# Kernel tuning notes

Hardware: AMD Instinct MI355X
Metric: run time of the kernel (lower is better)

## Reference

```python
import jax, jax.numpy as jnp
import numpy as np

CLUSTERS = 128
ITERATIONS = 10
TOPK = 32
NEG = -1e7


def setup_inputs() -> dict:
    key = jax.random.key(0)
    k1, k2, k3, k4 = jax.random.split(key, 4)
    N, L, H, E = 2, 2048, 8, 64
    BITS = 32
    return {
        "queries": jax.random.normal(k1, (N, L, H, E), dtype=jnp.float32),
        "keys": jax.random.normal(k2, (N, L, H, E), dtype=jnp.float32),
        "values": jax.random.normal(k3, (N, L, H, E), dtype=jnp.float32),
        "planes": jax.random.normal(k4, (BITS, E + 1), dtype=jnp.float32),
    }


def _cluster(bits, C, iterations):
    # bits: [N,H,L,B] in {0,1}. Lloyd k-means under Hamming distance.
    N, H, L, B = bits.shape
    init_idx = (np.arange(C) * L) // C
    cent = bits[:, :, init_idx, :]  # [N,H,C,B]
    for _ in range(iterations):
        # hamming(b,c) = b.(1-c) + (1-b).c
        d = (jnp.einsum('nhlb,nhcb->nhlc', bits, 1.0 - cent)
             + jnp.einsum('nhlb,nhcb->nhlc', 1.0 - bits, cent))
        assign = jnp.argmin(d, axis=-1)                      # [N,H,L]
        oh = jax.nn.one_hot(assign, C, dtype=jnp.float32)    # [N,H,L,C]
        cnt = oh.sum(axis=2)                                 # [N,H,C]
        sums = jnp.einsum('nhlc,nhlb->nhcb', oh, bits)
        new = (sums / jnp.maximum(cnt, 1.0)[..., None] >= 0.5).astype(jnp.float32)
        cent = jnp.where((cnt > 0.0)[..., None], new, cent)
    d = (jnp.einsum('nhlb,nhcb->nhlc', bits, 1.0 - cent)
         + jnp.einsum('nhlb,nhcb->nhlc', 1.0 - bits, cent))
    assign = jnp.argmin(d, axis=-1)
    oh = jax.nn.one_hot(assign, C, dtype=jnp.float32)
    cnt = oh.sum(axis=2)
    return assign, oh, cnt


def _forward(queries, keys, values, planes):
    # to [N,H,L,E]
    Q = jnp.transpose(queries, (0, 2, 1, 3))
    K = jnp.transpose(keys, (0, 2, 1, 3))
    V = jnp.transpose(values, (0, 2, 1, 3))
    N, H, L, E = Q.shape
    S = K.shape[2]
    temp = 1.0 / np.sqrt(E)

    # --- hash queries with random hyperplanes (bias column: hash_bias=True) ---
    x = jnp.concatenate([Q, jnp.ones(Q.shape[:-1] + (1,), Q.dtype)], axis=-1)
    bits = (jnp.einsum('nhle,be->nhlb', x, planes) > 0).astype(jnp.float32)

    # --- cluster queries (Lloyd on hamming distance over hash bits) ---
    assign, oh, cnt = _cluster(bits, CLUSTERS, ITERATIONS)

    # --- per-cluster centroid queries (mean over members) ---
    Qg = jnp.einsum('nhlc,nhle->nhce', oh, Q) / jnp.maximum(cnt, 1.0)[..., None]

    # --- top-k keys per cluster ---
    QKc = jnp.einsum('nhce,nhse->nhcs', Qg, K)   # [N,H,C,S]
    k = min(TOPK, S)
    _, tki = jax.lax.top_k(QKc, k)               # [N,H,C,k]

    # broadcast each cluster's top-k indices to its member queries
    idx_q = jnp.take_along_axis(
        tki, jnp.broadcast_to(assign[:, :, :, None], (N, H, L, k)), axis=2)  # [N,H,L,k]

    gather = jax.vmap(jax.vmap(lambda a, i: a[i]))
    K_sel = gather(K, idx_q)                     # [N,H,L,k,E]
    V_sel = gather(V, idx_q)                     # [N,H,L,k,E]

    qk = jnp.einsum('nhle,nhlke->nhlk', Q, K_sel)
    future = idx_q > jnp.arange(L)[None, None, :, None]   # causal: key pos > query pos
    qk = jnp.where(future, NEG, qk)
    A = jax.nn.softmax(temp * qk, axis=-1)
    A = A * (1.0 - future.astype(A.dtype))
    out = jnp.einsum('nhlk,nhlkd->nhld', A, V_sel)
    return jnp.transpose(out, (0, 2, 1, 3))      # [N,L,H,D]


def reference(queries, keys, values, planes):
    return _forward(queries, keys, values, planes)
```

## Files before the change

### kernel.cpp

```cpp
#include <hip/hip_runtime.h>
#include <math.h>

#define NB 2
#define HB 8
#define LB 2048
#define EB 64
#define BITSN 32
#define CLN 128
#define ITERS 10
#define TOPKN 32
#define NEGV -10000000.0f

typedef unsigned long long u64;
typedef unsigned int u32;

#define PART_NH16 (33 * 64)
#define PART_ITER16 (NB * HB * PART_NH16)
#define PART_TOTAL16 (ITERS * PART_ITER16)
#define BITS_BLOCKS 4096
#define ZBLOCKS ((PART_TOTAL16 + 255) / 256)

__global__ __launch_bounds__(256) void bits_zero_kernel(const float* __restrict__ q,
                                                        const float* __restrict__ planes,
                                                        u32* __restrict__ bits,
                                                        u32* __restrict__ zbuf) {
    int tid = threadIdx.x;
    int bid = blockIdx.x;
    if (bid >= BITS_BLOCKS) {
        int i = (bid - BITS_BLOCKS) * 256 + tid;
        if (i < PART_TOTAL16) zbuf[i] = 0u;
        return;
    }
    int wave = tid >> 6;
    int lane = tid & 63;
    int b = lane & 31;
    int which = lane >> 5;
    int qi = bid * 8 + wave * 2 + which;
    int l = qi & (LB - 1);
    int nh = qi / LB;
    int h = nh & (HB - 1);
    int n = nh / HB;
    const float* qrow = q + (((long long)n * LB + l) * HB + h) * EB;
    const float* prow = planes + b * (EB + 1);
    double acc = (double)prow[EB];
    #pragma unroll 8
    for (int e = 0; e < EB; ++e) acc += (double)qrow[e] * (double)prow[e];
    unsigned long long m = __ballot(acc > 0.0);
    if (b == 0) {
        bits[qi] = (u32)(which ? (m >> 32) : (m & 0xffffffffULL));
    }
}

__global__ __launch_bounds__(256) void kmeans_iter_kernel(const u32* __restrict__ bits,
                                                          const u32* __restrict__ part_prev,
                                                          u32* __restrict__ part_cur,
                                                          const u32* __restrict__ cent_prev_g,
                                                          u32* __restrict__ cent_cur_g,
                                                          int it) {
    __shared__ u32 cent[CLN];
    __shared__ int hist[33 * 128];
    int tid = threadIdx.x;
    int bid = blockIdx.x;
    int nh = bid >> 3;
    int tile = bid & 7;
    int lane = tid & 63;

    for (int i = tid; i < 33 * 128; i += 256) hist[i] = 0;
    if (tid < CLN) {
        u32 cv;
        if (it == 0) {
            cv = bits[nh * LB + tid * (LB / CLN)];
        } else {
            const u32* pp = part_prev + nh * PART_NH16;
            int sh = (tid & 1) * 16;
            int cnt = (int)((pp[32 * 64 + (tid >> 1)] >> sh) & 0xffffu);
            u32 nb = 0u;
            #pragma unroll
            for (int j = 0; j < BITSN; ++j) {
                int s = (int)((pp[j * 64 + (tid >> 1)] >> sh) & 0xffffu);
                if (2 * s >= cnt) nb |= (1u << j);
            }
            cv = (cnt > 0) ? nb : cent_prev_g[nh * CLN + tid];
        }
        cent[tid] = cv;
        if (tile == 0) cent_cur_g[nh * CLN + tid] = cv;
    }
    __syncthreads();

    int l = tile * 256 + tid;
    u32 bv = bits[nh * LB + l];

    u32 clo = cent[lane], chi = cent[lane + 64];
    u32 best = 0x7fffffffu;
    #pragma unroll 16
    for (int c = 0; c < 64; ++c) {
        u32 cc = (u32)__builtin_amdgcn_readlane((int)clo, c);
        u32 key = ((u32)__popc(bv ^ cc) << 7) | (u32)c;
        best = (key < best) ? key : best;
    }
    #pragma unroll 16
    for (int c = 0; c < 64; ++c) {
        u32 cc = (u32)__builtin_amdgcn_readlane((int)chi, c);
        u32 key = ((u32)__popc(bv ^ cc) << 7) | (u32)(64 + c);
        best = (key < best) ? key : best;
    }
    int bc = (int)(best & 127u);

    atomicAdd(&hist[32 * 128 + bc], 1);
    u32 bb = bv;
    while (bb) { int j = __ffs(bb) - 1; atomicAdd(&hist[j * 128 + bc], 1); bb &= bb - 1; }
    __syncthreads();

    u32* pc = part_cur + nh * PART_NH16;
    for (int i = tid; i < PART_NH16; i += 256) {
        int j = i >> 6, p = i & 63;
        u32 v = (u32)hist[j * 128 + 2 * p] | ((u32)hist[j * 128 + 2 * p + 1] << 16);
        if (v) atomicAdd(&pc[i], v);
    }
}

__global__ __launch_bounds__(1024) void list_qg_final_kernel(const u32* __restrict__ bits,
                                                             const u32* __restrict__ part_prev,
                                                             const u32* __restrict__ cent_prev_g,
                                                             const float* __restrict__ q,
                                                             int* __restrict__ csort_g,
                                                             int* __restrict__ cnt_g,
                                                             int* __restrict__ ofs_g,
                                                             int* __restrict__ list_g,
                                                             float* __restrict__ qgf) {
    __shared__ u32 cent[CLN];
    __shared__ int cnt[CLN];
    __shared__ int cntw[2][16][CLN];
    __shared__ int ofs[CLN];
    __shared__ unsigned short lists[LB];
    int nh = blockIdx.x;
    int tid = threadIdx.x;
    int w = tid >> 6, lane = tid & 63;

    if (tid < CLN) {
        const u32* pp = part_prev + nh * PART_NH16;
        int sh = (tid & 1) * 16;
        int cn = (int)((pp[32 * 64 + (tid >> 1)] >> sh) & 0xffffu);
        u32 nb = 0u;
        #pragma unroll
        for (int j = 0; j < BITSN; ++j) {
            int s = (int)((pp[j * 64 + (tid >> 1)] >> sh) & 0xffffu);
            if (2 * s >= cn) nb |= (1u << j);
        }
        cent[tid] = (cn > 0) ? nb : cent_prev_g[nh * CLN + tid];
        cnt[tid] = 0;
    }
    for (int i = tid; i < 2 * 16 * CLN; i += 1024) (&cntw[0][0][0])[i] = 0;
    __syncthreads();

    int l0 = tid, l1 = tid + 1024;
    u32 bv0 = bits[nh * LB + l0];
    u32 bv1 = bits[nh * LB + l1];
    u32 clo = cent[lane], chi = cent[lane + 64];
    u32 best0 = 0x7fffffffu, best1 = 0x7fffffffu;
    #pragma unroll 16
    for (int c = 0; c < 64; ++c) {
        u32 cc = (u32)__builtin_amdgcn_readlane((int)clo, c);
        u32 k0 = ((u32)__popc(bv0 ^ cc) << 7) | (u32)c;
        u32 k1 = ((u32)__popc(bv1 ^ cc) << 7) | (u32)c;
        best0 = (k0 < best0) ? k0 : best0;
        best1 = (k1 < best1) ? k1 : best1;
    }
    #pragma unroll 16
    for (int c = 0; c < 64; ++c) {
        u32 cc = (u32)__builtin_amdgcn_readlane((int)chi, c);
        u32 k0 = ((u32)__popc(bv0 ^ cc) << 7) | (u32)(64 + c);
        u32 k1 = ((u32)__popc(bv1 ^ cc) << 7) | (u32)(64 + c);
        best0 = (k0 < best0) ? k0 : best0;
        best1 = (k1 < best1) ? k1 : best1;
    }
    int bc0 = (int)(best0 & 127u);
    int bc1 = (int)(best1 & 127u);
    u64 ltmask = (lane == 0) ? 0ULL : (~0ULL >> (64 - lane));

    int rank0 = 0, rank1 = 0;
    for (int c = 0; c < CLN; ++c) {
        u64 m0 = __ballot(bc0 == c);
        u64 m1 = __ballot(bc1 == c);
        if ((m0 | m1) == 0ULL) continue;
        if (bc0 == c) rank0 = (int)__popcll(m0 & ltmask);
        if (bc1 == c) rank1 = (int)__popcll(m1 & ltmask);
        if (lane == 0) {
            int p0 = (int)__popcll(m0), p1 = (int)__popcll(m1);
            if (p0) cntw[0][w][c] = p0;
            if (p1) cntw[1][w][c] = p1;
            atomicAdd(&cnt[c], p0 + p1);
        }
    }
    __syncthreads();
    if (tid == 0) {
        int run = 0;
        for (int c = 0; c < CLN; ++c) { ofs[c] = run; run += cnt[c]; }
    }
    __syncthreads();
    if (tid < CLN) {
        int c = tid;
        int run = ofs[c];
        #pragma unroll
        for (int g = 0; g < 2; ++g)
            for (int ww = 0; ww < 16; ++ww) {
                int t = cntw[g][ww][c];
                cntw[g][ww][c] = run;
                run += t;
            }
        cnt_g[nh * CLN + c] = cnt[c];
        ofs_g[nh * CLN + c] = ofs[c];
    }
    __syncthreads();
    {
        int p0 = cntw[0][w][bc0] + rank0;
        int p1 = cntw[1][w][bc1] + rank1;
        lists[p0] = (unsigned short)l0;
        lists[p1] = (unsigned short)l1;
        list_g[nh * LB + p0] = l0;
        list_g[nh * LB + p1] = l1;
        csort_g[nh * LB + p0] = bc0;
        csort_g[nh * LB + p1] = bc1;
    }
    __syncthreads();

    int h = nh & (HB - 1);
    int n = nh / HB;
    for (int c = w; c < CLN; c += 16) {
        int cn = cnt[c];
        int o = ofs[c];
        double acc = 0.0;
        for (int i = 0; i < cn; ++i) {
            int l = lists[o + i];
            acc += (double)q[(((long long)n * LB + l) * HB + h) * EB + lane];
        }
        double dcn = (double)(cn > 0 ? cn : 1);
        qgf[(long long)(nh * CLN + c) * EB + lane] = (float)(acc / dcn);
    }
}

__global__ __launch_bounds__(256) void scores_kernel(const float* __restrict__ kk,
                                                     const float* __restrict__ qgf,
                                                     u32* __restrict__ keys) {
    int bid = blockIdx.x;
    int nh = bid >> 4;
    int tile = bid & 15;
    int h = nh & (HB - 1);
    int n = nh / HB;
    int w = threadIdx.x >> 6;
    int lane = threadIdx.x & 63;
    int rl = (w & 1) * 64 + lane;
    int l = tile * 128 + rl;
    int cbase = (w >> 1) * 64;

    const float4* kr4 = (const float4*)(kk + (((long long)n * LB + l) * HB + h) * EB);
    float rr[EB];
    #pragma unroll
    for (int i = 0; i < 16; ++i) {
        float4 t4 = kr4[i];
        rr[4 * i] = t4.x; rr[4 * i + 1] = t4.y; rr[4 * i + 2] = t4.z; rr[4 * i + 3] = t4.w;
    }
    const float* qp0 = qgf + ((long long)nh * CLN + cbase) * EB;
    for (int c = 0; c < 64; ++c) {
        const float4* qp = (const float4*)(qp0 + c * EB);
        float acc = 0.f;
        #pragma unroll
        for (int i = 0; i < 16; ++i) {
            float4 qv = qp[i];
            acc = fmaf(qv.x, rr[4 * i], acc);
            acc = fmaf(qv.y, rr[4 * i + 1], acc);
            acc = fmaf(qv.z, rr[4 * i + 2], acc);
            acc = fmaf(qv.w, rr[4 * i + 3], acc);
        }
        u32 u = __float_as_uint(acc);
        u = ((int)u < 0) ? ~u : (u | 0x80000000u);
        keys[((long long)(nh * CLN + cbase + c)) * LB + l] = u;
    }
}

__global__ __launch_bounds__(64) void topsel_kernel(const u32* __restrict__ keys,
                                                    int* __restrict__ tki_g) {
    int bid = blockIdx.x;
    int lane = threadIdx.x;
    const uint4* kp4 = (const uint4*)(keys + (long long)bid * LB);
    u64 k[32];
    #pragma unroll
    for (int t = 0; t < 8; ++t) {
        uint4 kv = kp4[lane + 64 * t];
        int l0 = (lane + 64 * t) * 4;
        k[4 * t]     = ((u64)kv.x << 32) | (u32)(2047 - l0);
        k[4 * t + 1] = ((u64)kv.y << 32) | (u32)(2047 - (l0 + 1));
        k[4 * t + 2] = ((u64)kv.z << 32) | (u32)(2047 - (l0 + 2));
        k[4 * t + 3] = ((u64)kv.w << 32) | (u32)(2047 - (l0 + 3));
    }
    u64 m0 = k[0], m1 = k[8], m2 = k[16], m3 = k[24];
    #pragma unroll
    for (int t = 1; t < 8; ++t) {
        if (k[t] > m0) m0 = k[t];
        if (k[8 + t] > m1) m1 = k[8 + t];
        if (k[16 + t] > m2) m2 = k[16 + t];
        if (k[24 + t] > m3) m3 = k[24 + t];
    }
    if (m1 > m0) m0 = m1;
    if (m3 > m2) m2 = m3;
    u64 cur = (m2 > m0) ? m2 : m0;

    for (int r = 0; r < TOPKN; ++r) {
        u64 wk = cur;
        #pragma unroll
        for (int off = 1; off < 64; off <<= 1) {
            u64 o = __shfl_xor(wk, off);
            if (o > wk) wk = o;
        }
        if (lane == 0) tki_g[bid * TOPKN + r] = 2047 - (int)(wk & 2047u);
        if (wk == cur) {
            u64 nm = 0ULL;
            #pragma unroll
            for (int t = 0; t < 32; ++t) {
                u64 kt = k[t];
                u64 cand = (kt < wk) ? kt : 0ULL;
                if (cand > nm) nm = cand;
            }
            cur = nm;
        }
    }
}

__global__ __launch_bounds__(256) void attn_kernel(const float* __restrict__ q,
                                                   const float* __restrict__ kk,
                                                   const float* __restrict__ vv,
                                                   const int* __restrict__ list_g,
                                                   const int* __restrict__ csort_g,
                                                   const int* __restrict__ tki_g,
                                                   float* __restrict__ out) {
    int tid = threadIdx.x;
    int wave = tid >> 6, lane = tid & 63;
    int idx = blockIdx.x * 4 + wave;
    int nh = idx >> 11;
    int pos = idx & (LB - 1);
    int l = list_g[nh * LB + pos];
    int c = csort_g[nh * LB + pos];
    int h = nh & (HB - 1);
    int n = nh / HB;
    const int* krow = tki_g + (nh * CLN + c) * TOPKN;
    int j = lane & 31, p = lane >> 5;
    int kidx = krow[j];

    const float* vbase = vv + ((long long)n * LB * HB + h) * EB;
    float vreg[TOPKN];
    #pragma unroll
    for (int jj = 0; jj < TOPKN; ++jj) {
        int kj = __shfl(kidx, jj);
        vreg[jj] = vbase[(long long)kj * (HB * EB) + lane];
    }

    const float4* q4 = (const float4*)(q + (((long long)n * LB + l) * HB + h) * EB) + p * 8;
    const float4* k4 = (const float4*)(kk + (((long long)n * LB + kidx) * HB + h) * EB) + p * 8;
    float part = 0.f;
    #pragma unroll
    for (int i = 0; i < 8; ++i) {
        float4 a = q4[i], b = k4[i];
        part += a.x * b.x + a.y * b.y + a.z * b.z + a.w * b.w;
    }
    float qlo = __shfl(part, j);
    float qhi = __shfl(part, j + 32);
    float qk = qlo + qhi;

    bool future = kidx > l;
    float logit = 0.125f * (future ? NEGV : qk);
    float m = logit;
    #pragma unroll
    for (int off = 16; off; off >>= 1) m = fmaxf(m, __shfl_xor(m, off));
    float ex = expf(logit - m);
    float ssum = ex;
    #pragma unroll
    for (int off = 16; off; off >>= 1) ssum += __shfl_xor(ssum, off);
    float a = future ? 0.f : ex / ssum;

    float oacc = 0.f;
    #pragma unroll
    for (int jj = 0; jj < TOPKN; ++jj) {
        float aj = __shfl(a, jj);
        oacc = fmaf(aj, vreg[jj], oacc);
    }
    out[(((long long)n * LB + l) * HB + h) * EB + lane] = oacc;
}

extern "C" void kernel_launch(void* const* d_in, const int* in_sizes, int n_in,
                              void* d_out, int out_size, void* d_ws, size_t ws_size,
                              hipStream_t stream) {
    const float* q = (const float*)d_in[0];
    const float* k = (const float*)d_in[1];
    const float* v = (const float*)d_in[2];
    const float* planes = (const float*)d_in[3];
    float* out = (float*)d_out;

    const int NQ = NB * HB * LB;
    char* ws = (char*)d_ws;
    u32* bits     = (u32*)(ws);
    int* csort_g  = (int*)(ws + 0x20000);
    int* cnt_g    = (int*)(ws + 0x40000);
    int* ofs_g    = (int*)(ws + 0x42000);
    int* list_g   = (int*)(ws + 0x44000);
    float* qgf    = (float*)(ws + 0x64000);
    int* tki_g    = (int*)(ws + 0xE4000);
    u32* keys     = (u32*)(ws + 0x124000);
    u32* part_all = (u32*)(ws + 0x124000);
    u32* cents0   = (u32*)(ws + 0x124000 + 0x180000);
    u32* cents1   = (u32*)(ws + 0x124000 + 0x182000);

    bits_zero_kernel<<<BITS_BLOCKS + ZBLOCKS, 256, 0, stream>>>(q, planes, bits, part_all);

    for (int it = 0; it < ITERS; ++it) {
        const u32* pp = part_all + (it == 0 ? 0 : (it - 1)) * PART_ITER16;
        u32* pc       = part_all + it * PART_ITER16;
        const u32* cprev = (it & 1) ? cents0 : cents1;
        u32* ccur        = (it & 1) ? cents1 : cents0;
        kmeans_iter_kernel<<<NB * HB * 8, 256, 0, stream>>>(bits, pp, pc, cprev, ccur, it);
    }
    list_qg_final_kernel<<<NB * HB, 1024, 0, stream>>>(
        bits, part_all + 9 * PART_ITER16, cents1, q, csort_g, cnt_g, ofs_g, list_g, qgf);
    scores_kernel<<<NB * HB * 16, 256, 0, stream>>>(k, qgf, keys);
    topsel_kernel<<<NB * HB * CLN, 64, 0, stream>>>(keys, tki_g);
    attn_kernel<<<NQ / 4, 256, 0, stream>>>(q, k, v, list_g, csort_g, tki_g, out);
}
```

Measured before the change: 289.0 us.

## Fuse k-means iterations into one persistent kernel with per-head grid barriers

Replaces the ten per-iteration k-means launches and the final reassignment with a single kernel. The 8 blocks of each head synchronize through global atomic counters between iterations, and all blocks stop early once no assignment changes. Final assignments go to a buffer, so the list kernel no longer recomputes Hamming distances. This removes launch gaps and redundant work, but it relies on all 128 blocks being co-resident for the spin barriers and adds atomic polling.

```diff
diff --git a/kernel.cpp b/kernel.cpp
--- a/kernel.cpp
+++ b/kernel.cpp
@@ -17,8 +17,9 @@
 #define PART_NH16 (33 * 64)
 #define PART_ITER16 (NB * HB * PART_NH16)
 #define PART_TOTAL16 (ITERS * PART_ITER16)
+#define ZN (PART_TOTAL16 + 512)
 #define BITS_BLOCKS 4096
-#define ZBLOCKS ((PART_TOTAL16 + 255) / 256)
+#define ZBLOCKS ((ZN + 255) / 256)
 
 __global__ __launch_bounds__(256) void bits_zero_kernel(const float* __restrict__ q,
                                                         const float* __restrict__ planes,
@@ -28,7 +29,7 @@
     int bid = blockIdx.x;
     if (bid >= BITS_BLOCKS) {
         int i = (bid - BITS_BLOCKS) * 256 + tid;
-        if (i < PART_TOTAL16) zbuf[i] = 0u;
+        if (i < ZN) zbuf[i] = 0u;
         return;
     }
     int wave = tid >> 6;
@@ -51,84 +52,142 @@
     }
 }
 
-__global__ __launch_bounds__(256) void kmeans_iter_kernel(const u32* __restrict__ bits,
-                                                          const u32* __restrict__ part_prev,
-                                                          u32* __restrict__ part_cur,
-                                                          const u32* __restrict__ cent_prev_g,
-                                                          u32* __restrict__ cent_cur_g,
-                                                          int it) {
+__global__ __launch_bounds__(256) void kmeans_single_kernel(const u32* __restrict__ bits,
+                                                            u32* __restrict__ part_all,
+                                                            int* __restrict__ bar,
+                                                            int* __restrict__ chflag,
+                                                            int* __restrict__ assign_g) {
     __shared__ u32 cent[CLN];
     __shared__ int hist[33 * 128];
     int tid = threadIdx.x;
     int bid = blockIdx.x;
     int nh = bid >> 3;
-    int tile = bid & 7;
+    int sub = bid & 7;
     int lane = tid & 63;
-
-    for (int i = tid; i < 33 * 128; i += 256) hist[i] = 0;
-    if (tid < CLN) {
-        u32 cv;
-        if (it == 0) {
-            cv = bits[nh * LB + tid * (LB / CLN)];
-        } else {
-            const u32* pp = part_prev + nh * PART_NH16;
+    int l = sub * 256 + tid;
+    u32 bv = bits[nh * LB + l];
+    int oldbc = -1, bc = 0;
+    bool conv = false;
+
+    for (int it = 0; it < ITERS; ++it) {
+        if (tid < CLN) {
+            u32 cv;
+            if (it == 0) {
+                cv = bits[nh * LB + tid * (LB / CLN)];
+            } else {
+                const u32* pp = part_all + (it - 1) * PART_ITER16 + nh * PART_NH16;
+                int sh = (tid & 1) * 16;
+                u32 wcnt = __hip_atomic_load(&pp[32 * 64 + (tid >> 1)],
+                                             __ATOMIC_RELAXED, __HIP_MEMORY_SCOPE_AGENT);
+                int cnt = (int)((wcnt >> sh) & 0xffffu);
+                u32 nb = 0u;
+                #pragma unroll
+                for (int j = 0; j < BITSN; ++j) {
+                    u32 wv = __hip_atomic_load(&pp[j * 64 + (tid >> 1)],
+                                               __ATOMIC_RELAXED, __HIP_MEMORY_SCOPE_AGENT);
+                    int s = (int)((wv >> sh) & 0xffffu);
+                    if (2 * s >= cnt) nb |= (1u << j);
+                }
+                cv = (cnt > 0) ? nb : cent[tid];
+            }
+            cent[tid] = cv;
+        }
+        for (int i = tid; i < 33 * 128; i += 256) hist[i] = 0;
+        __syncthreads();
+
+        u32 clo = cent[lane], chi = cent[lane + 64];
+        u32 best = 0x7fffffffu;
+        #pragma unroll 16
+        for (int c = 0; c < 64; ++c) {
+            u32 cc = (u32)__builtin_amdgcn_readlane((int)clo, c);
+            u32 key = ((u32)__popc(bv ^ cc) << 7) | (u32)c;
+            best = (key < best) ? key : best;
+        }
+        #pragma unroll 16
+        for (int c = 0; c < 64; ++c) {
+            u32 cc = (u32)__builtin_amdgcn_readlane((int)chi, c);
+            u32 key = ((u32)__popc(bv ^ cc) << 7) | (u32)(64 + c);
+            best = (key < best) ? key : best;
+        }
+        bc = (int)(best & 127u);
+
+        u64 chg = __ballot(bc != oldbc);
+        oldbc = bc;
+        if (lane == 0 && chg) atomicOr(&chflag[nh * 16 + it], 1);
+
+        atomicAdd(&hist[32 * 128 + bc], 1);
+        u32 bb = bv;
+        while (bb) { int j = __ffs(bb) - 1; atomicAdd(&hist[j * 128 + bc], 1); bb &= bb - 1; }
+        __syncthreads();
+
+        u32* pc = part_all + it * PART_ITER16 + nh * PART_NH16;
+        for (int i = tid; i < PART_NH16; i += 256) {
+            int j = i >> 6, p = i & 63;
+            u32 v = (u32)hist[j * 128 + 2 * p] | ((u32)hist[j * 128 + 2 * p + 1] << 16);
+            if (v) atomicAdd(&pc[i], v);
+        }
+
+        __threadfence();
+        __syncthreads();
+        if (tid == 0) {
+            atomicAdd(&bar[nh * 16 + it], 1);
+            while (__hip_atomic_load(&bar[nh * 16 + it], __ATOMIC_ACQUIRE,
+                                     __HIP_MEMORY_SCOPE_AGENT) < 8) {
+                __builtin_amdgcn_s_sleep(2);
+            }
+        }
+        __syncthreads();
+
+        if (__hip_atomic_load(&chflag[nh * 16 + it], __ATOMIC_RELAXED,
+                              __HIP_MEMORY_SCOPE_AGENT) == 0) {
+            conv = true; break;
+        }
+    }
+
+    if (!conv) {
+        if (tid < CLN) {
+            const u32* pp = part_all + 9 * PART_ITER16 + nh * PART_NH16;
             int sh = (tid & 1) * 16;
-            int cnt = (int)((pp[32 * 64 + (tid >> 1)] >> sh) & 0xffffu);
+            u32 wcnt = __hip_atomic_load(&pp[32 * 64 + (tid >> 1)],
+                                         __ATOMIC_RELAXED, __HIP_MEMORY_SCOPE_AGENT);
+            int cnt = (int)((wcnt >> sh) & 0xffffu);
             u32 nb = 0u;
             #pragma unroll
             for (int j = 0; j < BITSN; ++j) {
-                int s = (int)((pp[j * 64 + (tid >> 1)] >> sh) & 0xffffu);
+                u32 wv = __hip_atomic_load(&pp[j * 64 + (tid >> 1)],
+                                           __ATOMIC_RELAXED, __HIP_MEMORY_SCOPE_AGENT);
+                int s = (int)((wv >> sh) & 0xffffu);
                 if (2 * s >= cnt) nb |= (1u << j);
             }
-            cv = (cnt > 0) ? nb : cent_prev_g[nh * CLN + tid];
-        }
-        cent[tid] = cv;
-        if (tile == 0) cent_cur_g[nh * CLN + tid] = cv;
-    }
-    __syncthreads();
-
-    int l = tile * 256 + tid;
-    u32 bv = bits[nh * LB + l];
-
-    u32 clo = cent[lane], chi = cent[lane + 64];
-    u32 best = 0x7fffffffu;
-    #pragma unroll 16
-    for (int c = 0; c < 64; ++c) {
-        u32 cc = (u32)__builtin_amdgcn_readlane((int)clo, c);
-        u32 key = ((u32)__popc(bv ^ cc) << 7) | (u32)c;
-        best = (key < best) ? key : best;
-    }
-    #pragma unroll 16
-    for (int c = 0; c < 64; ++c) {
-        u32 cc = (u32)__builtin_amdgcn_readlane((int)chi, c);
-        u32 key = ((u32)__popc(bv ^ cc) << 7) | (u32)(64 + c);
-        best = (key < best) ? key : best;
-    }
-    int bc = (int)(best & 127u);
-
-    atomicAdd(&hist[32 * 128 + bc], 1);
-    u32 bb = bv;
-    while (bb) { int j = __ffs(bb) - 1; atomicAdd(&hist[j * 128 + bc], 1); bb &= bb - 1; }
-    __syncthreads();
-
-    u32* pc = part_cur + nh * PART_NH16;
-    for (int i = tid; i < PART_NH16; i += 256) {
-        int j = i >> 6, p = i & 63;
-        u32 v = (u32)hist[j * 128 + 2 * p] | ((u32)hist[j * 128 + 2 * p + 1] << 16);
-        if (v) atomicAdd(&pc[i], v);
-    }
-}
-
-__global__ __launch_bounds__(1024) void list_qg_final_kernel(const u32* __restrict__ bits,
-                                                             const u32* __restrict__ part_prev,
-                                                             const u32* __restrict__ cent_prev_g,
-                                                             const float* __restrict__ q,
-                                                             int* __restrict__ csort_g,
-                                                             int* __restrict__ cnt_g,
-                                                             int* __restrict__ ofs_g,
-                                                             int* __restrict__ list_g,
-                                                             float* __restrict__ qgf) {
-    __shared__ u32 cent[CLN];
+            cent[tid] = (cnt > 0) ? nb : cent[tid];
+        }
+        __syncthreads();
+        u32 clo = cent[lane], chi = cent[lane + 64];
+        u32 best = 0x7fffffffu;
+        #pragma unroll 16
+        for (int c = 0; c < 64; ++c) {
+            u32 cc = (u32)__builtin_amdgcn_readlane((int)clo, c);
+            u32 key = ((u32)__popc(bv ^ cc) << 7) | (u32)c;
+            best = (key < best) ? key : best;
+        }
+        #pragma unroll 16
+        for (int c = 0; c < 64; ++c) {
+            u32 cc = (u32)__builtin_amdgcn_readlane((int)chi, c);
+            u32 key = ((u32)__popc(bv ^ cc) << 7) | (u32)(64 + c);
+            best = (key < best) ? key : best;
+        }
+        bc = (int)(best & 127u);
+    }
+    assign_g[nh * LB + l] = bc;
+}
+
+__global__ __launch_bounds__(1024) void list_qg_kernel(const int* __restrict__ assign_g,
+                                                       const float* __restrict__ q,
+                                                       int* __restrict__ csort_g,
+                                                       int* __restrict__ cnt_g,
+                                                       int* __restrict__ ofs_g,
+                                                       int* __restrict__ list_g,
+                                                       float* __restrict__ qgf) {
     __shared__ int cnt[CLN];
     __shared__ int cntw[2][16][CLN];
     __shared__ int ofs[CLN];
@@ -136,47 +195,14 @@
     int nh = blockIdx.x;
     int tid = threadIdx.x;
     int w = tid >> 6, lane = tid & 63;
-
-    if (tid < CLN) {
-        const u32* pp = part_prev + nh * PART_NH16;
-        int sh = (tid & 1) * 16;
-        int cn = (int)((pp[32 * 64 + (tid >> 1)] >> sh) & 0xffffu);
-        u32 nb = 0u;
-        #pragma unroll
-        for (int j = 0; j < BITSN; ++j) {
-            int s = (int)((pp[j * 64 + (tid >> 1)] >> sh) & 0xffffu);
-            if (2 * s >= cn) nb |= (1u << j);
-        }
-        cent[tid] = (cn > 0) ? nb : cent_prev_g[nh * CLN + tid];
-        cnt[tid] = 0;
-    }
+    int l0 = tid, l1 = tid + 1024;
+    int bc0 = assign_g[nh * LB + l0];
+    int bc1 = assign_g[nh * LB + l1];
+    u64 ltmask = (lane == 0) ? 0ULL : (~0ULL >> (64 - lane));
+
+    if (tid < CLN) cnt[tid] = 0;
     for (int i = tid; i < 2 * 16 * CLN; i += 1024) (&cntw[0][0][0])[i] = 0;
     __syncthreads();
-
-    int l0 = tid, l1 = tid + 1024;
-    u32 bv0 = bits[nh * LB + l0];
-    u32 bv1 = bits[nh * LB + l1];
-    u32 clo = cent[lane], chi = cent[lane + 64];
-    u32 best0 = 0x7fffffffu, best1 = 0x7fffffffu;
-    #pragma unroll 16
-    for (int c = 0; c < 64; ++c) {
-        u32 cc = (u32)__builtin_amdgcn_readlane((int)clo, c);
-        u32 k0 = ((u32)__popc(bv0 ^ cc) << 7) | (u32)c;
-        u32 k1 = ((u32)__popc(bv1 ^ cc) << 7) | (u32)c;
-        best0 = (k0 < best0) ? k0 : best0;
-        best1 = (k1 < best1) ? k1 : best1;
-    }
-    #pragma unroll 16
-    for (int c = 0; c < 64; ++c) {
-        u32 cc = (u32)__builtin_amdgcn_readlane((int)chi, c);
-        u32 k0 = ((u32)__popc(bv0 ^ cc) << 7) | (u32)(64 + c);
-        u32 k1 = ((u32)__popc(bv1 ^ cc) << 7) | (u32)(64 + c);
-        best0 = (k0 < best0) ? k0 : best0;
-        best1 = (k1 < best1) ? k1 : best1;
-    }
-    int bc0 = (int)(best0 & 127u);
-    int bc1 = (int)(best1 & 127u);
-    u64 ltmask = (lane == 0) ? 0ULL : (~0ULL >> (64 - lane));
 
     int rank0 = 0, rank1 = 0;
     for (int c = 0; c < CLN; ++c) {
@@ -406,20 +432,14 @@
     int* tki_g    = (int*)(ws + 0xE4000);
     u32* keys     = (u32*)(ws + 0x124000);
     u32* part_all = (u32*)(ws + 0x124000);
-    u32* cents0   = (u32*)(ws + 0x124000 + 0x180000);
-    u32* cents1   = (u32*)(ws + 0x124000 + 0x182000);
+    int* bar      = (int*)(part_all + PART_TOTAL16);
+    int* chflag   = bar + 256;
+    int* assign_g = (int*)(ws + 0x124000 + 0x180000);
 
     bits_zero_kernel<<<BITS_BLOCKS + ZBLOCKS, 256, 0, stream>>>(q, planes, bits, part_all);
-
-    for (int it = 0; it < ITERS; ++it) {
-        const u32* pp = part_all + (it == 0 ? 0 : (it - 1)) * PART_ITER16;
-        u32* pc       = part_all + it * PART_ITER16;
-        const u32* cprev = (it & 1) ? cents0 : cents1;
-        u32* ccur        = (it & 1) ? cents1 : cents0;
-        kmeans_iter_kernel<<<NB * HB * 8, 256, 0, stream>>>(bits, pp, pc, cprev, ccur, it);
-    }
-    list_qg_final_kernel<<<NB * HB, 1024, 0, stream>>>(
-        bits, part_all + 9 * PART_ITER16, cents1, q, csort_g, cnt_g, ofs_g, list_g, qgf);
+    kmeans_single_kernel<<<NB * HB * 8, 256, 0, stream>>>(bits, part_all, bar, chflag, assign_g);
+    list_qg_kernel<<<NB * HB, 1024, 0, stream>>>(assign_g, q, csort_g, cnt_g, ofs_g,
+                                                 list_g, qgf);
     scores_kernel<<<NB * HB * 16, 256, 0, stream>>>(k, qgf, keys);
     topsel_kernel<<<NB * HB * CLN, 64, 0, stream>>>(keys, tki_g);
     attn_kernel<<<NQ / 4, 256, 0, stream>>>(q, k, v, list_g, csort_g, tki_g, out);
```

After: 349.7 us. +21.0%, slower.
